# Kernel tuning notes

Measured on AMD Instinct MI355X. Metric: run time of the kernel, lower is better.

Reference implementation:

```python
import jax, jax.numpy as jnp
import numpy as np

T1 = 0.001
T2 = 0.5
ALPHA = 1.0
EPS = 1e-6


def setup_inputs() -> dict:
    key = jax.random.key(0)
    k1, k2, k3, k4, k5 = jax.random.split(key, 5)
    N, D, C, P = 1024, 1024, 32768, 128
    x = jax.random.normal(k1, (N, D), dtype=jnp.float32)
    # params.weight init: uniform(-0.05, 0.05); bias filled with 0 in torch, use small randn to exercise grads
    W = jax.random.uniform(k2, (C, D), dtype=jnp.float32, minval=-0.05, maxval=0.05)
    b = jax.random.normal(k3, (C,), dtype=jnp.float32) * 0.01
    rp = jax.random.normal(k4, (D + 1, P), dtype=jnp.float32)  # SimHash random projection (D+1, K*L)
    sample_ids = jax.random.randint(k5, (C,), 0, C, dtype=jnp.int64)  # LSH candidate set
    return {"x": x, "W": W, "b": b, "rp": rp, "sample_ids": sample_ids}


def reference(x, W, b, rp, sample_ids):
    N, D = x.shape
    C = W.shape[0]
    S = sample_ids.shape[0]
    # query_tolsh = cat(x, ones)
    q = jnp.concatenate([x, jnp.ones((N, 1), x.dtype)], axis=1)  # (N, D+1)
    # sparse embedding gather of candidate weights/bias
    sw = W[sample_ids]          # (S, D)
    sb = b[sample_ids]          # (S,)
    sample_product = x @ sw.T   # (N, S)
    sample_logits = sample_product + sb[None, :]
    # kthvalue-based thresholds (torch.kthvalue is 1-indexed, k-th smallest along last dim)
    t1_th = int(C * (1.0 - T1))
    t2_th = int(C * (1.0 - T2))
    sorted_prod = jnp.sort(sample_product, axis=-1)
    t1_ip = jnp.maximum(jnp.mean(sorted_prod[:, t1_th - 1]), 0.0)
    t2_ip = jnp.mean(sorted_prod[:, t2_th - 1])
    pos_mask = sample_product > t1_ip
    neg_mask = sample_product < t2_ip
    # triplet loss on hash-projected cosine similarity; p_x/p_weight/n_x/n_weight are detached in torch
    qd = jax.lax.stop_gradient(q)
    wcat = jax.lax.stop_gradient(jnp.concatenate([sw, sb[:, None]], axis=1))  # (S, D+1)
    qp = qd @ rp    # (N, P)
    wp = wcat @ rp  # (S, P)
    qn = qp / jnp.maximum(jnp.linalg.norm(qp, axis=-1, keepdims=True), EPS)
    wn = wp / jnp.maximum(jnp.linalg.norm(wp, axis=-1, keepdims=True), EPS)
    sim = qn @ wn.T  # (N, S) cosine similarity for every (query, candidate) pair
    # deterministic surrogate for the random-pairing hinge: masked mean sims
    pf = pos_mask.astype(sim.dtype)
    nf = neg_mask.astype(sim.dtype)
    sim_p = jnp.sum(sim * pf) / jnp.maximum(jnp.sum(pf), 1.0)
    sim_n = jnp.sum(sim * nf) / jnp.maximum(jnp.sum(nf), 1.0)
    triplet_loss = jnp.maximum(sim_n - sim_p + ALPHA, 0.0)
    return sample_logits, triplet_loss
```

## Files before the change

### kernel.cpp

```cpp
#include <hip/hip_runtime.h>


using short8v = __attribute__((ext_vector_type(8))) short;
using f32x4   = __attribute__((ext_vector_type(4))) float;

#define AS1C(p) ((const __attribute__((address_space(1))) void*)(p))
#define AS3(p)  ((__attribute__((address_space(3))) void*)(p))

__device__ __forceinline__ unsigned short f2bf(float f) {
  union { float f; unsigned u; } v; v.f = f;
  unsigned u = v.u;
  return (unsigned short)((u + 0x7FFFu + ((u >> 16) & 1u)) >> 16);
}
__device__ __forceinline__ float bf2f(unsigned short s) {
  return __uint_as_float(((unsigned)s) << 16);
}

__global__ __launch_bounds__(256) void k_gather(
    const float* __restrict__ W, const float* __restrict__ bb,
    const float* __restrict__ x, const int* __restrict__ ids,
    unsigned short* __restrict__ swb, float* __restrict__ sbg,
    unsigned short* __restrict__ xb) {
  const int t = threadIdx.x;
  const int blk = blockIdx.x;
  if (blk < 32768) {
    const int id = ids[blk];
    float4 v = *(const float4*)&W[(size_t)id * 1024 + t * 4];
    ushort4 o; o.x = f2bf(v.x); o.y = f2bf(v.y); o.z = f2bf(v.z); o.w = f2bf(v.w);
    *(ushort4*)&swb[(size_t)blk * 1024 + t * 4] = o;
    if (t == 0) sbg[blk] = bb[id];
  } else {
    const int r = blk - 32768;
    float4 v = *(const float4*)&x[(size_t)r * 1024 + t * 4];
    ushort4 o; o.x = f2bf(v.x); o.y = f2bf(v.y); o.z = f2bf(v.z); o.w = f2bf(v.w);
    *(ushort4*)&xb[(size_t)r * 1024 + t * 4] = o;
  }
}

__global__ __launch_bounds__(256) void k_qn(
    const float* __restrict__ x, const float* __restrict__ rp,
    unsigned short* __restrict__ qnb) {
  __shared__ float xs[4][1024];
  __shared__ float part[4][2];
  const int t = threadIdx.x;
  const int r0 = blockIdx.x * 4;
#pragma unroll
  for (int i = 0; i < 4; ++i) {
    int idx = i * 256 + t, rr = idx >> 8, c4 = idx & 255;
    *(float4*)&xs[rr][c4 * 4] = *(const float4*)&x[(size_t)(r0 + rr) * 1024 + c4 * 4];
  }
  __syncthreads();
  const int col = t & 127, rsel = t >> 7;
  float a0 = 0.f, a1 = 0.f;
  for (int k = 0; k < 1024; k += 4) {
    float4 xa = *(const float4*)&xs[rsel][k];
    float4 xbv = *(const float4*)&xs[rsel + 2][k];
    float av[4] = {xa.x, xa.y, xa.z, xa.w};
    float bv[4] = {xbv.x, xbv.y, xbv.z, xbv.w};
#pragma unroll
    for (int j = 0; j < 4; ++j) {
      float rv = rp[(size_t)(k + j) * 128 + col];
      a0 += av[j] * rv;
      a1 += bv[j] * rv;
    }
  }
  { float rv = rp[(size_t)1024 * 128 + col]; a0 += rv; a1 += rv; }
  float s0 = a0 * a0, s1 = a1 * a1;
#pragma unroll
  for (int m = 1; m < 64; m <<= 1) { s0 += __shfl_xor(s0, m, 64); s1 += __shfl_xor(s1, m, 64); }
  if ((t & 63) == 0) { part[t >> 6][0] = s0; part[t >> 6][1] = s1; }
  __syncthreads();
  float n0 = part[2 * rsel][0] + part[2 * rsel + 1][0];
  float n1 = part[2 * rsel][1] + part[2 * rsel + 1][1];
  qnb[(size_t)(r0 + rsel) * 128 + col]     = f2bf(a0 / fmaxf(sqrtf(n0), 1e-6f));
  qnb[(size_t)(r0 + rsel + 2) * 128 + col] = f2bf(a1 / fmaxf(sqrtf(n1), 1e-6f));
}

__device__ __forceinline__ void stage_sw(const unsigned short* g, int lda,
                                         unsigned short* l, int t) {
#pragma unroll
  for (int i = 0; i < 2; ++i) {
    const int idx = i * 256 + t;
    const int row = idx >> 2;
    const int c = (idx & 3) ^ ((row >> 1) & 3);
    const unsigned short* gp = g + (size_t)row * lda + c * 8;
    __builtin_amdgcn_global_load_lds(AS1C(gp), AS3(l + idx * 8), 16, 0, 0);
  }
}

__device__ __forceinline__ void stage_rp(const float* __restrict__ rp, int k0,
                                         unsigned short* l, int t) {
#pragma unroll
  for (int ii = 0; ii < 4; ++ii) {
    int idx = ii * 256 + t;
    int kk = idx & 31, c4 = idx >> 5;
    float4 v = *(const float4*)&rp[(size_t)(k0 + kk) * 128 + c4 * 4];
    l[(c4 * 4 + 0) * 32 + kk] = f2bf(v.x);
    l[(c4 * 4 + 1) * 32 + kk] = f2bf(v.y);
    l[(c4 * 4 + 2) * 32 + kk] = f2bf(v.z);
    l[(c4 * 4 + 3) * 32 + kk] = f2bf(v.w);
  }
}

__global__ __launch_bounds__(256) void k_wn(
    const unsigned short* __restrict__ swb, const float* __restrict__ rp,
    const float* __restrict__ sbg, unsigned short* __restrict__ wnb) {
  __shared__ unsigned short As[2][128 * 32];
  __shared__ unsigned short Bs[2][128 * 32];
  __shared__ float nbuf[2][128];
  const int t = threadIdx.x;
  const int r0 = blockIdx.x * 128;
  const unsigned short* Ag = swb + (size_t)r0 * 1024;
  f32x4 acc[4][4];
#pragma unroll
  for (int m = 0; m < 4; ++m)
#pragma unroll
    for (int n = 0; n < 4; ++n) acc[m][n] = f32x4{0.f, 0.f, 0.f, 0.f};
  stage_sw(Ag, 1024, &As[0][0], t);
  stage_rp(rp, 0, &Bs[0][0], t);
  const int l = t & 63, w = t >> 6, wm = w >> 1, wn = w & 1;
  const int lr = l & 15, lk = l >> 4;
  const int kch = lk * 8;
  const int ach = (lk ^ ((lr >> 1) & 3)) * 8;
  for (int kt = 0; kt < 32; ++kt) {
    const int cur = kt & 1;
    __syncthreads();
    if (kt + 1 < 32) {
      stage_sw(Ag + (kt + 1) * 32, 1024, &As[cur ^ 1][0], t);
      stage_rp(rp, (kt + 1) * 32, &Bs[cur ^ 1][0], t);
    }
    short8v a[4], b[4];
#pragma unroll
    for (int m = 0; m < 4; ++m) a[m] = *(const short8v*)&As[cur][(wm * 64 + m * 16 + lr) * 32 + ach];
#pragma unroll
    for (int n = 0; n < 4; ++n) b[n] = *(const short8v*)&Bs[cur][(wn * 64 + n * 16 + lr) * 32 + kch];
#pragma unroll
    for (int m = 0; m < 4; ++m)
#pragma unroll
      for (int n = 0; n < 4; ++n)
        acc[m][n] = __builtin_amdgcn_mfma_f32_16x16x32_bf16(a[m], b[n], acc[m][n], 0, 0, 0);
  }
  const float* rpl = rp + (size_t)1024 * 128;
  float sb_r[4][4];
#pragma unroll
  for (int m = 0; m < 4; ++m)
#pragma unroll
    for (int i = 0; i < 4; ++i)
      sb_r[m][i] = sbg[r0 + wm * 64 + m * 16 + lk * 4 + i];
#pragma unroll
  for (int n = 0; n < 4; ++n) {
    const int gc = wn * 64 + n * 16 + lr;
    const float rl = rpl[gc];
#pragma unroll
    for (int m = 0; m < 4; ++m)
#pragma unroll
      for (int i = 0; i < 4; ++i) acc[m][n][i] += sb_r[m][i] * rl;
  }
#pragma unroll
  for (int m = 0; m < 4; ++m)
#pragma unroll
    for (int i = 0; i < 4; ++i) {
      float s = 0.f;
#pragma unroll
      for (int n = 0; n < 4; ++n) s += acc[m][n][i] * acc[m][n][i];
#pragma unroll
      for (int msk = 1; msk < 16; msk <<= 1) s += __shfl_xor(s, msk, 64);
      if (lr == 0) nbuf[wn][wm * 64 + m * 16 + lk * 4 + i] = s;
    }
  __syncthreads();
#pragma unroll
  for (int m = 0; m < 4; ++m)
#pragma unroll
    for (int i = 0; i < 4; ++i) {
      const int lrow = wm * 64 + m * 16 + lk * 4 + i;
      const float n2 = nbuf[0][lrow] + nbuf[1][lrow];
      const float sc = 1.f / fmaxf(sqrtf(n2), 1e-6f);
#pragma unroll
      for (int n = 0; n < 4; ++n) {
        const int gc = wn * 64 + n * 16 + lr;
        wnb[(size_t)(r0 + lrow) * 128 + gc] = f2bf(acc[m][n][i] * sc);
      }
    }
}

__global__ __launch_bounds__(256) void k_gemm_main(
    const unsigned short* __restrict__ A, const unsigned short* __restrict__ B,
    const float* __restrict__ sbg, float* __restrict__ out) {
  __shared__ unsigned short As[2][128 * 32];
  __shared__ unsigned short Bs[2][128 * 32];
  const int t = threadIdx.x;
  const int lb = (blockIdx.x & 7) * 256 + (blockIdx.x >> 3);
  const int bm = lb & 7, bn = lb >> 3;
  const unsigned short* Ag = A + (size_t)bm * 128 * 1024;
  const unsigned short* Bg = B + (size_t)bn * 128 * 1024;
  f32x4 acc[2][8];
#pragma unroll
  for (int m = 0; m < 2; ++m)
#pragma unroll
    for (int n = 0; n < 8; ++n) acc[m][n] = f32x4{0.f, 0.f, 0.f, 0.f};
  stage_sw(Ag, 1024, &As[0][0], t);
  stage_sw(Bg, 1024, &Bs[0][0], t);
  const int l = t & 63, w = t >> 6;
  const int lr = l & 15, lk = l >> 4;
  const int ach = (lk ^ ((lr >> 1) & 3)) * 8;
  for (int kt = 0; kt < 32; ++kt) {
    const int cur = kt & 1;
    __syncthreads();
    if (kt + 1 < 32) {
      stage_sw(Ag + (kt + 1) * 32, 1024, &As[cur ^ 1][0], t);
      stage_sw(Bg + (kt + 1) * 32, 1024, &Bs[cur ^ 1][0], t);
    }
    short8v a[2], b[8];
#pragma unroll
    for (int m = 0; m < 2; ++m)
      a[m] = *(const short8v*)&As[cur][(w * 32 + m * 16 + lr) * 32 + ach];
#pragma unroll
    for (int n = 0; n < 8; ++n)
      b[n] = *(const short8v*)&Bs[cur][(n * 16 + lr) * 32 + ach];
#pragma unroll
    for (int m = 0; m < 2; ++m)
#pragma unroll
      for (int n = 0; n < 8; ++n)
        acc[m][n] = __builtin_amdgcn_mfma_f32_16x16x32_bf16(a[m], b[n], acc[m][n], 0, 0, 0);
  }
  const int rb = bm * 128 + w * 32, cb = bn * 128;
#pragma unroll
  for (int n = 0; n < 8; ++n) {
    const int gc = cb + n * 16 + lr;
    const float bias = sbg[gc];
#pragma unroll
    for (int m = 0; m < 2; ++m)
#pragma unroll
      for (int i = 0; i < 4; ++i) {
        const int gr = rb + m * 16 + lk * 4 + i;
        out[(size_t)gr * 32768 + gc] = acc[m][n][i] + bias;
      }
  }
}

__global__ __launch_bounds__(256) void k_hist(
    const float* __restrict__ logits, const float* __restrict__ sbg,
    float* __restrict__ kth1, float* __restrict__ kth2) {
  __shared__ unsigned short rowm[32768];
  __shared__ unsigned hist[2048];
  __shared__ unsigned scanbuf[256];
  __shared__ unsigned hsub[64];
  __shared__ int res[4];
  const int t = threadIdx.x, row = blockIdx.x;
  for (int i = t; i < 2048; i += 256) hist[i] = 0u;
  if (t < 64) hsub[t] = 0u;
  __syncthreads();
  const float* lp = logits + (size_t)row * 32768;
  for (int c = t * 4; c < 32768; c += 1024) {
    const float4 lv = *(const float4*)&lp[c];
    const float4 sb4 = *(const float4*)&sbg[c];
    const float pr[4] = {lv.x - sb4.x, lv.y - sb4.y, lv.z - sb4.z, lv.w - sb4.w};
    unsigned short mm[4];
#pragma unroll
    for (int j = 0; j < 4; ++j) {
      const unsigned short bbf = f2bf(pr[j]);
      const unsigned m = (bbf & 0x8000u) ? (0xFFFFu ^ (unsigned)bbf)
                                         : ((unsigned)bbf | 0x8000u);
      mm[j] = (unsigned short)m;
      atomicAdd(&hist[m >> 5], 1u);
    }
    *(ushort4*)&rowm[c] = make_ushort4(mm[0], mm[1], mm[2], mm[3]);
  }
  __syncthreads();
  {
    unsigned s = 0;
#pragma unroll
    for (int j = 0; j < 8; ++j) s += hist[t * 8 + j];
    scanbuf[t] = s;
    __syncthreads();
    unsigned x = s;
    for (int off = 1; off < 256; off <<= 1) {
      unsigned y = (t >= off) ? scanbuf[t - off] : 0u;
      __syncthreads();
      x += y; scanbuf[t] = x;
      __syncthreads();
    }
    unsigned run = x - s;
    const unsigned K1R = 32734u, K2R = 16383u;
#pragma unroll
    for (int j = 0; j < 8; ++j) {
      unsigned c = hist[t * 8 + j];
      if (K1R >= run && K1R < run + c) { res[0] = t * 8 + j; res[1] = (int)(K1R - run); }
      if (K2R >= run && K2R < run + c) { res[2] = t * 8 + j; res[3] = (int)(K2R - run); }
      run += c;
    }
  }
  __syncthreads();
  const unsigned bin1 = (unsigned)res[0], r1 = (unsigned)res[1];
  const unsigned bin2 = (unsigned)res[2], r2 = (unsigned)res[3];
  for (int c = t; c < 32768; c += 256) {
    const unsigned m = rowm[c];
    const unsigned bq = m >> 5;
    if (bq == bin1) atomicAdd(&hsub[m & 31], 1u);
    if (bq == bin2) atomicAdd(&hsub[32 + (m & 31)], 1u);
  }
  __syncthreads();
  if (t == 0) {
    unsigned a_ = 0; int sub1 = 31;
    for (int j = 0; j < 32; ++j) { if (r1 < a_ + hsub[j]) { sub1 = j; break; } a_ += hsub[j]; }
    a_ = 0; int sub2 = 31;
    for (int j = 0; j < 32; ++j) { if (r2 < a_ + hsub[32 + j]) { sub2 = j; break; } a_ += hsub[32 + j]; }
    const unsigned m1 = (bin1 << 5) | (unsigned)sub1;
    const unsigned m2 = (bin2 << 5) | (unsigned)sub2;
    kth1[row] = bf2f((unsigned short)((m1 & 0x8000u) ? (m1 & 0x7FFFu) : (0xFFFFu ^ m1)));
    kth2[row] = bf2f((unsigned short)((m2 & 0x8000u) ? (m2 & 0x7FFFu) : (0xFFFFu ^ m2)));
  }
}

__global__ __launch_bounds__(256) void k_thresh(
    const float* __restrict__ k1, const float* __restrict__ k2,
    float* __restrict__ scal) {
  const int t = threadIdx.x;
  float s1 = 0.f, s2 = 0.f;
  for (int i = t; i < 1024; i += 256) { s1 += k1[i]; s2 += k2[i]; }
#pragma unroll
  for (int m = 1; m < 64; m <<= 1) { s1 += __shfl_xor(s1, m, 64); s2 += __shfl_xor(s2, m, 64); }
  __shared__ float p[4][2];
  if ((t & 63) == 0) { p[t >> 6][0] = s1; p[t >> 6][1] = s2; }
  __syncthreads();
  if (t == 0) {
    float t1 = (p[0][0] + p[1][0] + p[2][0] + p[3][0]) / 1024.f;
    float t2 = (p[0][1] + p[1][1] + p[2][1] + p[3][1]) / 1024.f;
    scal[0] = fmaxf(t1, 0.f);
    scal[1] = t2;
  }
}

__global__ __launch_bounds__(256) void k_sim(
    const unsigned short* __restrict__ A, const unsigned short* __restrict__ B,
    const float* __restrict__ logits, const float* __restrict__ sbg,
    const float* __restrict__ scal, float4* __restrict__ part) {
  __shared__ unsigned short As[128 * 32];
  __shared__ unsigned short Bs[128 * 32];
  __shared__ unsigned short simb[128 * 128];
  __shared__ float red[4][4];
  const int t = threadIdx.x;
  const int bm = blockIdx.x & 7, bn = blockIdx.x >> 3;
  const unsigned short* Ag = A + (size_t)bm * 128 * 128;
  const unsigned short* Bg = B + (size_t)bn * 128 * 128;
  f32x4 acc[4][4];
#pragma unroll
  for (int m = 0; m < 4; ++m)
#pragma unroll
    for (int n = 0; n < 4; ++n) acc[m][n] = f32x4{0.f, 0.f, 0.f, 0.f};
  const int l = t & 63, w = t >> 6, wm = w >> 1, wn = w & 1;
  const int lr = l & 15, lk = l >> 4;
  const int ach = (lk ^ ((lr >> 1) & 3)) * 8;
  for (int kt = 0; kt < 4; ++kt) {
    stage_sw(Ag + kt * 32, 128, &As[0], t);
    stage_sw(Bg + kt * 32, 128, &Bs[0], t);
    __syncthreads();
    short8v a[4], b[4];
#pragma unroll
    for (int m = 0; m < 4; ++m) a[m] = *(const short8v*)&As[(wm * 64 + m * 16 + lr) * 32 + ach];
#pragma unroll
    for (int n = 0; n < 4; ++n) b[n] = *(const short8v*)&Bs[(wn * 64 + n * 16 + lr) * 32 + ach];
#pragma unroll
    for (int m = 0; m < 4; ++m)
#pragma unroll
      for (int n = 0; n < 4; ++n)
        acc[m][n] = __builtin_amdgcn_mfma_f32_16x16x32_bf16(a[m], b[n], acc[m][n], 0, 0, 0);
    __syncthreads();
  }
#pragma unroll
  for (int m = 0; m < 4; ++m)
#pragma unroll
    for (int n = 0; n < 4; ++n) {
      const int col = wn * 64 + n * 16 + lr;
#pragma unroll
      for (int i = 0; i < 4; ++i) {
        const int row = wm * 64 + m * 16 + lk * 4 + i;
        simb[row * 128 + col] = f2bf(acc[m][n][i]);
      }
    }
  __syncthreads();
  const float t1 = scal[0], t2 = scal[1];
  const int rb0 = bm * 128, cb0 = bn * 128;
  float ps = 0.f, pc = 0.f, ns = 0.f, nc = 0.f;
#pragma unroll
  for (int it = 0; it < 16; ++it) {
    const int idx = it * 256 + t;
    const int rr = idx >> 5;
    const int c4 = idx & 31;
    const float4 lv = *(const float4*)&logits[(size_t)(rb0 + rr) * 32768 + cb0 + c4 * 4];
    const float4 sb4 = *(const float4*)&sbg[cb0 + c4 * 4];
    const ushort4 sv = *(const ushort4*)&simb[rr * 128 + c4 * 4];
    const float pr[4] = {lv.x - sb4.x, lv.y - sb4.y, lv.z - sb4.z, lv.w - sb4.w};
    const float sm[4] = {bf2f(sv.x), bf2f(sv.y), bf2f(sv.z), bf2f(sv.w)};
#pragma unroll
    for (int j = 0; j < 4; ++j) {
      if (pr[j] > t1) { ps += sm[j]; pc += 1.f; }
      if (pr[j] < t2) { ns += sm[j]; nc += 1.f; }
    }
  }
#pragma unroll
  for (int m = 1; m < 64; m <<= 1) {
    ps += __shfl_xor(ps, m, 64); pc += __shfl_xor(pc, m, 64);
    ns += __shfl_xor(ns, m, 64); nc += __shfl_xor(nc, m, 64);
  }
  if (l == 0) { red[w][0] = ps; red[w][1] = pc; red[w][2] = ns; red[w][3] = nc; }
  __syncthreads();
  if (t == 0) {
    float4 o;
    o.x = red[0][0] + red[1][0] + red[2][0] + red[3][0];
    o.y = red[0][1] + red[1][1] + red[2][1] + red[3][1];
    o.z = red[0][2] + red[1][2] + red[2][2] + red[3][2];
    o.w = red[0][3] + red[1][3] + red[2][3] + red[3][3];
    part[blockIdx.x] = o;
  }
}

__global__ __launch_bounds__(256) void k_final(
    const float4* __restrict__ part, float* __restrict__ out) {
  __shared__ float red[4][4];
  const int t = threadIdx.x;
  float ps = 0.f, pc = 0.f, ns = 0.f, nc = 0.f;
  for (int i = t; i < 2048; i += 256) {
    float4 v = part[i];
    ps += v.x; pc += v.y; ns += v.z; nc += v.w;
  }
#pragma unroll
  for (int m = 1; m < 64; m <<= 1) {
    ps += __shfl_xor(ps, m, 64); pc += __shfl_xor(pc, m, 64);
    ns += __shfl_xor(ns, m, 64); nc += __shfl_xor(nc, m, 64);
  }
  const int w = t >> 6;
  if ((t & 63) == 0) { red[w][0] = ps; red[w][1] = pc; red[w][2] = ns; red[w][3] = nc; }
  __syncthreads();
  if (t == 0) {
    float tps = red[0][0] + red[1][0] + red[2][0] + red[3][0];
    float tpc = red[0][1] + red[1][1] + red[2][1] + red[3][1];
    float tns = red[0][2] + red[1][2] + red[2][2] + red[3][2];
    float tnc = red[0][3] + red[1][3] + red[2][3] + red[3][3];
    float sp = tps / fmaxf(tpc, 1.f);
    float sn = tns / fmaxf(tnc, 1.f);
    out[33554432] = fmaxf(sn - sp + 1.f, 0.f);
  }
}

extern "C" void kernel_launch(void* const* d_in, const int* in_sizes, int n_in,
                              void* d_out, int out_size, void* d_ws, size_t ws_size,
                              hipStream_t stream) {
  const float* x  = (const float*)d_in[0];
  const float* W  = (const float*)d_in[1];
  const float* b  = (const float*)d_in[2];
  const float* rp = (const float*)d_in[3];
  const int*  ids = (const int*)d_in[4];
  float* out = (float*)d_out;
  char* ws = (char*)d_ws;

  unsigned short* swb = (unsigned short*)(ws);
  unsigned short* xb  = (unsigned short*)(ws + 67108864);
  float*          sbg = (float*)(ws + 69206016);
  unsigned short* qnb = (unsigned short*)(ws + 69337088);
  unsigned short* wnb = (unsigned short*)(ws + 69599232);
  float*         kth1 = (float*)(ws + 78004224);
  float*         kth2 = (float*)(ws + 78008320);
  float*         scal = (float*)(ws + 78012416);
  float4*        part = (float4*)(ws + 78016512);

  k_gather   <<<33792, 256, 0, stream>>>(W, b, x, ids, swb, sbg, xb);
  k_qn       <<<256,   256, 0, stream>>>(x, rp, qnb);
  k_wn       <<<256,   256, 0, stream>>>(swb, rp, sbg, wnb);
  k_gemm_main<<<2048,  256, 0, stream>>>(xb, swb, sbg, out);
  k_hist     <<<1024,  256, 0, stream>>>(out, sbg, kth1, kth2);
  k_thresh   <<<1,     256, 0, stream>>>(kth1, kth2, scal);
  k_sim      <<<2048,  256, 0, stream>>>(qnb, wnb, out, sbg, scal, part);
  k_final    <<<1,     256, 0, stream>>>(part, out);
}
```

Before: 321.9 us.

## Triple-buffer main GEMM LDS staging with async global_load_lds and vmcnt waits

Switches the main logits GEMM from double to triple buffered LDS tiles. Tiles are prefetched two K-steps ahead with direct global-to-LDS loads, and fine-grained vmcnt waits plus a single barrier replace the per-iteration __syncthreads. The goal is to hide global memory latency behind MFMA work. In exchange it uses more shared memory per block, which may lower occupancy, and it relies on careful vmcnt counting being correct.

```diff
diff --git a/kernel.cpp b/kernel.cpp
--- a/kernel.cpp
+++ b/kernel.cpp
@@ -186,43 +186,66 @@
 __global__ __launch_bounds__(256) void k_gemm_main(
     const unsigned short* __restrict__ A, const unsigned short* __restrict__ B,
     const float* __restrict__ sbg, float* __restrict__ out) {
-  __shared__ unsigned short As[2][128 * 32];
-  __shared__ unsigned short Bs[2][128 * 32];
+  __shared__ unsigned short As[3][128 * 32];
+  __shared__ unsigned short Bs[3][128 * 32];
   const int t = threadIdx.x;
   const int lb = (blockIdx.x & 7) * 256 + (blockIdx.x >> 3);
   const int bm = lb & 7, bn = lb >> 3;
   const unsigned short* Ag = A + (size_t)bm * 128 * 1024;
   const unsigned short* Bg = B + (size_t)bn * 128 * 1024;
+
+  auto stage = [&](int kt) {
+    unsigned short* la = &As[kt % 3][0];
+    unsigned short* lbp = &Bs[kt % 3][0];
+    const unsigned short* ga = Ag + kt * 32;
+    const unsigned short* gb = Bg + kt * 32;
+#pragma unroll
+    for (int i = 0; i < 2; ++i) {
+      const int idx = i * 256 + t;
+      const int row = idx >> 2;
+      const int c = (idx & 3) ^ ((row >> 1) & 3);
+      __builtin_amdgcn_global_load_lds(AS1C(ga + (size_t)row * 1024 + c * 8),
+                                       AS3(la + idx * 8), 16, 0, 0);
+      __builtin_amdgcn_global_load_lds(AS1C(gb + (size_t)row * 1024 + c * 8),
+                                       AS3(lbp + idx * 8), 16, 0, 0);
+    }
+  };
+
   f32x4 acc[2][8];
 #pragma unroll
   for (int m = 0; m < 2; ++m)
 #pragma unroll
     for (int n = 0; n < 8; ++n) acc[m][n] = f32x4{0.f, 0.f, 0.f, 0.f};
-  stage_sw(Ag, 1024, &As[0][0], t);
-  stage_sw(Bg, 1024, &Bs[0][0], t);
+
   const int l = t & 63, w = t >> 6;
   const int lr = l & 15, lk = l >> 4;
   const int ach = (lk ^ ((lr >> 1) & 3)) * 8;
+
+  stage(0); stage(1);
+  asm volatile("s_waitcnt vmcnt(4)" ::: "memory");
+  __builtin_amdgcn_s_barrier();
+
   for (int kt = 0; kt < 32; ++kt) {
-    const int cur = kt & 1;
-    __syncthreads();
-    if (kt + 1 < 32) {
-      stage_sw(Ag + (kt + 1) * 32, 1024, &As[cur ^ 1][0], t);
-      stage_sw(Bg + (kt + 1) * 32, 1024, &Bs[cur ^ 1][0], t);
-    }
+    if (kt + 2 < 32) stage(kt + 2);
+    const unsigned short* Ac = &As[kt % 3][0];
+    const unsigned short* Bc = &Bs[kt % 3][0];
     short8v a[2], b[8];
 #pragma unroll
     for (int m = 0; m < 2; ++m)
-      a[m] = *(const short8v*)&As[cur][(w * 32 + m * 16 + lr) * 32 + ach];
+      a[m] = *(const short8v*)&Ac[(w * 32 + m * 16 + lr) * 32 + ach];
 #pragma unroll
     for (int n = 0; n < 8; ++n)
-      b[n] = *(const short8v*)&Bs[cur][(n * 16 + lr) * 32 + ach];
+      b[n] = *(const short8v*)&Bc[(n * 16 + lr) * 32 + ach];
 #pragma unroll
     for (int m = 0; m < 2; ++m)
 #pragma unroll
       for (int n = 0; n < 8; ++n)
         acc[m][n] = __builtin_amdgcn_mfma_f32_16x16x32_bf16(a[m], b[n], acc[m][n], 0, 0, 0);
-  }
+    if (kt + 2 < 32)       asm volatile("s_waitcnt vmcnt(4)" ::: "memory");
+    else if (kt + 2 == 32) asm volatile("s_waitcnt vmcnt(0)" ::: "memory");
+    __builtin_amdgcn_s_barrier();
+  }
+
   const int rb = bm * 128 + w * 32, cb = bn * 128;
 #pragma unroll
   for (int n = 0; n < 8; ++n) {
```

Result: slower. 329.1 us (+2.2%).
